# Kernel tuning notes

Measured on AMD Instinct MI355X. Metric: run time of the kernel, lower is better.

The kernel has to match this reference:

```python
import jax, jax.numpy as jnp
import numpy as np

EPS = 1e-5  # torch InstanceNorm2d default eps

def conv1x1(x, w, b):
    # x: [B,C,H,W], w: [O,C], b: [O]
    return jnp.einsum('bchw,oc->bohw', x, w) + b[None, :, None, None]

def instance_norm(x):
    # InstanceNorm2d(affine=False): normalize per-sample, per-channel over H,W
    mean = jnp.mean(x, axis=(2, 3), keepdims=True)
    var = jnp.var(x, axis=(2, 3), keepdims=True)
    return (x - mean) * jax.lax.rsqrt(var + EPS)

def proj(x, w, b):
    return jax.nn.relu(instance_norm(conv1x1(x, w, b)))

def setup_inputs() -> dict:
    key = jax.random.key(0)
    ks = jax.random.split(key, 9)
    B, C, Ci, H, W = 16, 256, 128, 64, 64
    s_in = 1.0 / np.sqrt(C)
    s_mid = 1.0 / np.sqrt(Ci)
    return {
        'x': jax.random.normal(ks[0], (B, C, H, W), jnp.float32),
        'g_w': jax.random.normal(ks[1], (Ci, C), jnp.float32) * s_in,
        'g_b': jax.random.normal(ks[2], (Ci,), jnp.float32) * s_in,
        'theta_w': jax.random.normal(ks[3], (Ci, C), jnp.float32) * s_in,
        'theta_b': jax.random.normal(ks[4], (Ci,), jnp.float32) * s_in,
        'phi_w': jax.random.normal(ks[5], (Ci, C), jnp.float32) * s_in,
        'phi_b': jax.random.normal(ks[6], (Ci,), jnp.float32) * s_in,
        'W_w': jax.random.normal(ks[7], (C, Ci), jnp.float32) * s_mid,
        'W_b': jax.random.normal(ks[8], (C,), jnp.float32) * s_mid,
    }

def reference(x, g_w, g_b, theta_w, theta_b, phi_w, phi_b, W_w, W_b):
    B, C, H, W = x.shape
    Ci = g_w.shape[0]
    N = H * W
    g_x = proj(x, g_w, g_b).reshape(B, Ci, N)        # [B,Ci,N]
    theta_x = proj(x, theta_w, theta_b).reshape(B, Ci, N)
    phi_x = proj(x, phi_w, phi_b).reshape(B, Ci, N)
    # channel-attention Gram matrix [B,Ci,Ci], softmax over last dim
    f = jnp.einsum('bin,bjn->bij', theta_x, phi_x)
    attn = jax.nn.softmax(f, axis=2)
    y = jnp.einsum('bij,bjn->bin', attn, g_x)        # [B,Ci,N]
    # replicate torch permute(0,2,1).contiguous().view(B,Ci,H,W)
    y = jnp.transpose(y, (0, 2, 1)).reshape(B, Ci, H, W)
    y = instance_norm(conv1x1(y, W_w, W_b))
    return y + x
```

## Files before the change

kernel.cpp:

```cpp
#include <hip/hip_runtime.h>

#define DEVINL __device__ __forceinline__

typedef __attribute__((ext_vector_type(8))) short bf8v;
typedef __attribute__((ext_vector_type(4))) float f32x4;
typedef __attribute__((ext_vector_type(8))) unsigned short us8;
typedef __attribute__((ext_vector_type(4))) unsigned short us4;

DEVINL unsigned short f2bf(float f) {
  unsigned int u = __builtin_bit_cast(unsigned int, f);
  u += 0x7fffu + ((u >> 16) & 1u);
  return (unsigned short)(u >> 16);
}
DEVINL unsigned short f2bf_trunc(float f) {
  return (unsigned short)(__builtin_bit_cast(unsigned int, f) >> 16);
}
DEVINL float bf2f(unsigned short h) {
  unsigned int u = ((unsigned int)h) << 16;
  return __builtin_bit_cast(float, u);
}

__global__ __launch_bounds__(512, 2)
void proj_gemm(const unsigned short* __restrict__ wall_hi,
               const unsigned short* __restrict__ wall_lo,
               const float* __restrict__ x,
               unsigned short* __restrict__ zr_hi, unsigned short* __restrict__ zr_lo,
               float* __restrict__ partials)
{
  __shared__ __align__(16) unsigned short As_hi[384 * 72];
  __shared__ __align__(16) unsigned short As_lo[256 * 72];
  __shared__ __align__(16) unsigned short Bs_hi[128 * 72];
  __shared__ __align__(16) unsigned short Bs_lo[128 * 72];

  const int t = threadIdx.x;
  const int lane = t & 63;
  const int wave = t >> 6;
  const int wm = wave >> 1, wn = wave & 1;
  const int lr = lane & 15, lk = lane >> 4;
  const int b = blockIdx.z;
  const int bx = blockIdx.x;
  const int nbase = bx * 128;
  const float* xs = x + (long)b * 256 * 4096;

  const int nl = t & 127, cg = t >> 7;
  float xv[16];

  f32x4 acc[6][4];
#pragma unroll
  for (int i = 0; i < 6; ++i)
#pragma unroll
    for (int j = 0; j < 4; ++j) acc[i][j] = (f32x4)0.0f;

#pragma unroll
  for (int i = 0; i < 16; ++i)
    xv[i] = xs[(long)(cg * 16 + i) * 4096 + nbase + nl];

  for (int kt = 0; kt < 4; ++kt) {
    const int k0 = kt * 64;
#pragma unroll
    for (int i = 0; i < 6; ++i) {
      const int q = i * 512 + t;
      const int row = q >> 3, c = q & 7;
      *(us8*)&As_hi[row * 72 + c * 8] = *(const us8*)&wall_hi[(long)row * 256 + k0 + c * 8];
    }
#pragma unroll
    for (int i = 0; i < 4; ++i) {
      const int q = i * 512 + t;
      const int row = q >> 3, c = q & 7;
      *(us8*)&As_lo[row * 72 + c * 8] = *(const us8*)&wall_lo[(long)row * 256 + k0 + c * 8];
    }
#pragma unroll
    for (int ch = 0; ch < 2; ++ch) {
      us8 h8, l8;
#pragma unroll
      for (int e = 0; e < 8; ++e) {
        const float v = xv[ch * 8 + e];
        const unsigned short hb = f2bf(v);
        h8[e] = hb;
        l8[e] = f2bf_trunc(v - bf2f(hb));
      }
      *(us8*)&Bs_hi[nl * 72 + cg * 16 + ch * 8] = h8;
      *(us8*)&Bs_lo[nl * 72 + cg * 16 + ch * 8] = l8;
    }
    __syncthreads();

    if (kt < 3) {
      const int kn = (kt + 1) * 64;
#pragma unroll
      for (int i = 0; i < 16; ++i)
        xv[i] = xs[(long)(kn + cg * 16 + i) * 4096 + nbase + nl];
    }

#pragma unroll
    for (int ks = 0; ks < 2; ++ks) {
      const int ko = ks * 32 + lk * 8;
      bf8v bh[4], bl[4];
#pragma unroll
      for (int ni = 0; ni < 4; ++ni) {
        const int r = (wn * 64 + ni * 16 + lr) * 72 + ko;
        bh[ni] = *(const bf8v*)&Bs_hi[r];
        bl[ni] = *(const bf8v*)&Bs_lo[r];
      }
#pragma unroll
      for (int mi = 0; mi < 6; ++mi) {
        const int fr = mi * 4 + wm;
        const int r = (fr * 16 + lr) * 72 + ko;
        const bf8v ah = *(const bf8v*)&As_hi[r];
        if (fr < 16) {
          const bf8v al = *(const bf8v*)&As_lo[r];
#pragma unroll
          for (int ni = 0; ni < 4; ++ni) {
            acc[mi][ni] = __builtin_amdgcn_mfma_f32_16x16x32_bf16(bh[ni], ah, acc[mi][ni], 0, 0, 0);
            acc[mi][ni] = __builtin_amdgcn_mfma_f32_16x16x32_bf16(bl[ni], ah, acc[mi][ni], 0, 0, 0);
            acc[mi][ni] = __builtin_amdgcn_mfma_f32_16x16x32_bf16(bh[ni], al, acc[mi][ni], 0, 0, 0);
          }
        } else {
#pragma unroll
          for (int ni = 0; ni < 4; ++ni)
            acc[mi][ni] = __builtin_amdgcn_mfma_f32_16x16x32_bf16(bh[ni], ah, acc[mi][ni], 0, 0, 0);
        }
      }
    }
    __syncthreads();
  }

  float* sbuf = (float*)As_hi;
#pragma unroll
  for (int mi = 0; mi < 6; ++mi) {
    float s = 0.f, ss = 0.f;
#pragma unroll
    for (int ni = 0; ni < 4; ++ni)
#pragma unroll
      for (int r = 0; r < 4; ++r) {
        const float v = acc[mi][ni][r];
        s += v; ss += v * v;
      }
    const int fr = mi * 4 + wm;
    const int slot = ((fr * 16 + lr) * 8 + (wn * 4 + lk)) * 2;
    sbuf[slot] = s; sbuf[slot + 1] = ss;
  }
  __syncthreads();
  if (t < 384) {
    float s = 0.f, ss = 0.f;
#pragma unroll
    for (int w = 0; w < 8; ++w) {
      s += sbuf[(t * 8 + w) * 2];
      ss += sbuf[(t * 8 + w) * 2 + 1];
    }
    const long pidx = ((long)bx * 6144 + b * 384 + t) * 2;
    partials[pidx] = s; partials[pidx + 1] = ss;
  }

#pragma unroll
  for (int mi = 0; mi < 6; ++mi)
#pragma unroll
    for (int ni = 0; ni < 4; ++ni) {
      const int gm = (mi * 4 + wm) * 16 + lr;
      const int gn = nbase + wn * 64 + ni * 16 + lk * 4;
      const long o = ((long)b * 384 + gm) * 4096 + gn;
      us4 hv, lv;
#pragma unroll
      for (int r = 0; r < 4; ++r) {
        const float v = acc[mi][ni][r];
        const unsigned short h = f2bf(v);
        hv[r] = h;
        lv[r] = f2bf_trunc(v - bf2f(h));
      }
      *(us4*)&zr_hi[o] = hv;
      if (gm < 256) *(us4*)&zr_lo[o] = lv;
    }
}

__global__ __launch_bounds__(256)
void stats_reduce(const float* __restrict__ partials, float* __restrict__ stats)
{
  const int row = blockIdx.x * 256 + threadIdx.x;
  float s = 0.f, ss = 0.f;
#pragma unroll
  for (int k = 0; k < 32; ++k) {
    s += partials[((long)k * 6144 + row) * 2];
    ss += partials[((long)k * 6144 + row) * 2 + 1];
  }
  const float mean = s * (1.f / 4096.f);
  const float var = ss * (1.f / 4096.f) - mean * mean;
  const float rs = rsqrtf(fmaxf(var, 0.f) + 1e-5f);
  stats[row * 2] = rs;
  stats[row * 2 + 1] = -mean * rs;
}

__global__ __launch_bounds__(256, 4)
void fgemm_norm(const unsigned short* __restrict__ zr_hi, const unsigned short* __restrict__ zr_lo,
                const float* __restrict__ stats, float* __restrict__ fpart)
{
  __shared__ __align__(16) unsigned short As_hi[128 * 72];
  __shared__ __align__(16) unsigned short As_lo[128 * 72];
  __shared__ __align__(16) unsigned short Bs_hi[128 * 72];
  __shared__ __align__(16) unsigned short Bs_lo[128 * 72];

  const int t = threadIdx.x;
  const int lane = t & 63;
  const int wave = t >> 6;
  const int wm = wave >> 1, wn = wave & 1;
  const int lr = lane & 15, lk = lane >> 4;
  const int zb = blockIdx.z >> 5, z1 = blockIdx.z & 31;
  const int koff = z1 * 128;

  f32x4 acc[4][4];
#pragma unroll
  for (int i = 0; i < 4; ++i)
#pragma unroll
    for (int j = 0; j < 4; ++j) acc[i][j] = (f32x4)0.0f;

  for (int kt = 0; kt < 2; ++kt) {
    const int k0 = koff + kt * 64;
#pragma unroll
    for (int i = 0; i < 4; ++i) {
      const int q = i * 256 + t;
      const int row = q >> 3, c = q & 7;
#pragma unroll
      for (int op = 0; op < 2; ++op) {
        const int grow = zb * 384 + op * 128 + row;
        const long g = (long)grow * 4096 + k0 + c * 8;
        const us8 h = *(const us8*)&zr_hi[g];
        const us8 l = *(const us8*)&zr_lo[g];
        const float rs = stats[grow * 2];
        const float nmrs = stats[grow * 2 + 1];
        us8 oh, ol;
#pragma unroll
        for (int e = 0; e < 8; ++e) {
          const float v = bf2f(h[e]) + bf2f(l[e]);
          const float nv = fmaxf(__builtin_fmaf(v, rs, nmrs), 0.f);
          const unsigned short hb = f2bf(nv);
          oh[e] = hb;
          ol[e] = f2bf_trunc(nv - bf2f(hb));
        }
        unsigned short* dh = op ? Bs_hi : As_hi;
        unsigned short* dl = op ? Bs_lo : As_lo;
        *(us8*)&dh[row * 72 + c * 8] = oh;
        *(us8*)&dl[row * 72 + c * 8] = ol;
      }
    }
    __syncthreads();
#pragma unroll
    for (int ks = 0; ks < 2; ++ks) {
      const int ko = ks * 32 + lk * 8;
      bf8v ah[4], bh[4], al[4], bl[4];
#pragma unroll
      for (int mi = 0; mi < 4; ++mi) {
        const int r = (wm * 64 + mi * 16 + lr) * 72 + ko;
        ah[mi] = *(const bf8v*)&As_hi[r];
        al[mi] = *(const bf8v*)&As_lo[r];
      }
#pragma unroll
      for (int ni = 0; ni < 4; ++ni) {
        const int r = (wn * 64 + ni * 16 + lr) * 72 + ko;
        bh[ni] = *(const bf8v*)&Bs_hi[r];
        bl[ni] = *(const bf8v*)&Bs_lo[r];
      }
#pragma unroll
      for (int mi = 0; mi < 4; ++mi)
#pragma unroll
        for (int ni = 0; ni < 4; ++ni) {
          acc[mi][ni] = __builtin_amdgcn_mfma_f32_16x16x32_bf16(bh[ni], ah[mi], acc[mi][ni], 0, 0, 0);
          acc[mi][ni] = __builtin_amdgcn_mfma_f32_16x16x32_bf16(bl[ni], ah[mi], acc[mi][ni], 0, 0, 0);
          acc[mi][ni] = __builtin_amdgcn_mfma_f32_16x16x32_bf16(bh[ni], al[mi], acc[mi][ni], 0, 0, 0);
        }
    }
    __syncthreads();
  }

  const long cOff = ((long)zb * 32 + z1) * 16384;
#pragma unroll
  for (int mi = 0; mi < 4; ++mi)
#pragma unroll
    for (int ni = 0; ni < 4; ++ni) {
      const int gm = wm * 64 + mi * 16 + lr;
      const int gn = wn * 64 + ni * 16 + lk * 4;
      *(f32x4*)&fpart[cOff + (long)gm * 128 + gn] = acc[mi][ni];
    }
}

__global__ __launch_bounds__(256, 2)
void gemm_y(const unsigned short* __restrict__ Ah0, const unsigned short* __restrict__ Bh0,
            unsigned short* __restrict__ Cout,
            int lda, int ldb, int ldc, int ksteps, int z1count,
            long aS1, long aS2, long bS1, long bS2, long cS1, long cS2)
{
  __shared__ __align__(16) unsigned short As_hi[128 * 72];
  __shared__ __align__(16) unsigned short Bs_hi[128 * 72];

  const int t = threadIdx.x;
  const int lane = t & 63;
  const int wave = t >> 6;
  const int wm = wave >> 1, wn = wave & 1;
  const int lr = lane & 15, lk = lane >> 4;

  const int z = blockIdx.z;
  const int zb = z / z1count, z1 = z - zb * z1count;
  const unsigned short* Ah = Ah0 + zb * aS2 + z1 * aS1;
  const unsigned short* Bh = Bh0 + zb * bS2 + z1 * bS1;
  const long cOff = zb * cS2 + z1 * cS1;

  f32x4 acc[4][4];
#pragma unroll
  for (int i = 0; i < 4; ++i)
#pragma unroll
    for (int j = 0; j < 4; ++j) acc[i][j] = (f32x4)0.0f;

  for (int kt = 0; kt < ksteps; ++kt) {
    const int k0 = kt * 64;
#pragma unroll
    for (int i = 0; i < 4; ++i) {
      const int q = i * 256 + t;
      const int row = q >> 3, c = q & 7;
      const int lo = row * 72 + c * 8;
      *(us8*)&As_hi[lo] = *(const us8*)&Ah[(long)row * lda + k0 + c * 8];
      *(us8*)&Bs_hi[lo] = *(const us8*)&Bh[(long)row * ldb + k0 + c * 8];
    }
    __syncthreads();
#pragma unroll
    for (int ks = 0; ks < 2; ++ks) {
      const int ko = ks * 32 + lk * 8;
      bf8v ah[4], bh[4];
#pragma unroll
      for (int mi = 0; mi < 4; ++mi)
        ah[mi] = *(const bf8v*)&As_hi[(wm * 64 + mi * 16 + lr) * 72 + ko];
#pragma unroll
      for (int ni = 0; ni < 4; ++ni)
        bh[ni] = *(const bf8v*)&Bs_hi[(wn * 64 + ni * 16 + lr) * 72 + ko];
#pragma unroll
      for (int mi = 0; mi < 4; ++mi)
#pragma unroll
        for (int ni = 0; ni < 4; ++ni)
          acc[mi][ni] = __builtin_amdgcn_mfma_f32_16x16x32_bf16(bh[ni], ah[mi], acc[mi][ni], 0, 0, 0);
    }
    __syncthreads();
  }

#pragma unroll
  for (int mi = 0; mi < 4; ++mi)
#pragma unroll
    for (int ni = 0; ni < 4; ++ni) {
      const int gm = wm * 64 + mi * 16 + lr;
      const int gn = wn * 64 + ni * 16 + lk * 4;
      const f32x4 v = acc[mi][ni];
      us4 o;
#pragma unroll
      for (int r = 0; r < 4; ++r) o[r] = f2bf(v[r]);
      *(us4*)&Cout[cOff + (long)gm * ldc + gn] = o;
    }
}

__global__ __launch_bounds__(256, 2)
void conv2_gemm(const unsigned short* __restrict__ w2h,
                const unsigned short* __restrict__ y4T,
                unsigned short* __restrict__ z2b)
{
  __shared__ __align__(16) unsigned short As_hi[256 * 72];
  __shared__ __align__(16) unsigned short Bs_hi[128 * 72];

  const int t = threadIdx.x;
  const int lane = t & 63;
  const int wave = t >> 6;
  const int wm = wave >> 1, wn = wave & 1;
  const int lr = lane & 15, lk = lane >> 4;
  const int b = blockIdx.z;
  const int nbase = blockIdx.x * 128;
  const unsigned short* Bh = y4T + (long)b * 4096 * 128 + (long)nbase * 128;

  f32x4 acc[8][4];
#pragma unroll
  for (int i = 0; i < 8; ++i)
#pragma unroll
    for (int j = 0; j < 4; ++j) acc[i][j] = (f32x4)0.0f;

  for (int kt = 0; kt < 2; ++kt) {
    const int k0 = kt * 64;
#pragma unroll
    for (int i = 0; i < 8; ++i) {
      const int q = i * 256 + t;
      const int row = q >> 3, c = q & 7;
      *(us8*)&As_hi[row * 72 + c * 8] = *(const us8*)&w2h[(long)row * 128 + k0 + c * 8];
    }
#pragma unroll
    for (int i = 0; i < 4; ++i) {
      const int q = i * 256 + t;
      const int row = q >> 3, c = q & 7;
      *(us8*)&Bs_hi[row * 72 + c * 8] = *(const us8*)&Bh[(long)row * 128 + k0 + c * 8];
    }
    __syncthreads();
#pragma unroll
    for (int ks = 0; ks < 2; ++ks) {
      const int ko = ks * 32 + lk * 8;
      bf8v ah[8], bh[4];
#pragma unroll
      for (int mi = 0; mi < 8; ++mi)
        ah[mi] = *(const bf8v*)&As_hi[(wm * 128 + mi * 16 + lr) * 72 + ko];
#pragma unroll
      for (int ni = 0; ni < 4; ++ni)
        bh[ni] = *(const bf8v*)&Bs_hi[(wn * 64 + ni * 16 + lr) * 72 + ko];
#pragma unroll
      for (int mi = 0; mi < 8; ++mi)
#pragma unroll
        for (int ni = 0; ni < 4; ++ni)
          acc[mi][ni] = __builtin_amdgcn_mfma_f32_16x16x32_bf16(bh[ni], ah[mi], acc[mi][ni], 0, 0, 0);
    }
    __syncthreads();
  }

#pragma unroll
  for (int mi = 0; mi < 8; ++mi)
#pragma unroll
    for (int ni = 0; ni < 4; ++ni) {
      const int gm = wm * 128 + mi * 16 + lr;
      const int gn = nbase + wn * 64 + ni * 16 + lk * 4;
      const f32x4 v = acc[mi][ni];
      us4 o;
#pragma unroll
      for (int r = 0; r < 4; ++r) o[r] = f2bf(v[r]);
      *(us4*)&z2b[((long)b * 256 + gm) * 4096 + gn] = o;
    }
}

__global__ __launch_bounds__(256)
void prep_weights(const float* __restrict__ g_w, const float* __restrict__ th_w,
                  const float* __restrict__ ph_w, const float* __restrict__ W_w,
                  unsigned short* __restrict__ wall_hi, unsigned short* __restrict__ wall_lo,
                  unsigned short* __restrict__ w2h)
{
  const int i = blockIdx.x * 256 + threadIdx.x;
  float v;
  if (i < 32768) v = th_w[i];
  else if (i < 65536) v = ph_w[i - 32768];
  else v = g_w[i - 65536];
  const unsigned short h = f2bf(v);
  wall_hi[i] = h;
  if (i < 65536) wall_lo[i] = f2bf_trunc(v - bf2f(h));
  if (i < 32768) w2h[i] = f2bf(W_w[i]);
}

__global__ __launch_bounds__(256)
void norm_transpose_g(const unsigned short* __restrict__ zr_hi,
                      const float* __restrict__ stats,
                      unsigned short* __restrict__ gT)
{
  __shared__ unsigned short T[64 * 136];
  const int b = blockIdx.y, n0 = blockIdx.x * 64;
  const int t = threadIdx.x;
  const int c = t >> 1, part = t & 1;
  const int grow = b * 384 + 256 + c;
  const float rs = stats[grow * 2];
  const float nmrs = stats[grow * 2 + 1];
  const long off = (long)grow * 4096 + n0 + part * 32;
#pragma unroll
  for (int j = 0; j < 4; ++j) {
    const us8 h = *(const us8*)&zr_hi[off + j * 8];
#pragma unroll
    for (int e = 0; e < 8; ++e) {
      const float v = bf2f(h[e]);
      const float nv = fmaxf(__builtin_fmaf(v, rs, nmrs), 0.f);
      T[(part * 32 + j * 8 + e) * 136 + c] = f2bf(nv);
    }
  }
  __syncthreads();
  const int nl = t >> 2, q = t & 3;
  const long obase = ((long)b * 4096 + n0 + nl) * 128 + q * 32;
#pragma unroll
  for (int k = 0; k < 4; ++k) {
    us8 o;
#pragma unroll
    for (int e = 0; e < 8; ++e) o[e] = T[nl * 136 + q * 32 + k * 8 + e];
    *(us8*)&gT[obase + k * 8] = o;
  }
}

__global__ __launch_bounds__(64)
void softmax_attn(const float* __restrict__ fpart, unsigned short* __restrict__ attn)
{
  const int row = blockIdx.x;
  const int b = row >> 7, i = row & 127;
  const int t = threadIdx.x;
  float v0 = 0.f, v1 = 0.f;
#pragma unroll
  for (int kc = 0; kc < 32; ++kc) {
    const float* p = fpart + ((long)(b * 32 + kc)) * 16384 + i * 128;
    v0 += p[t];
    v1 += p[t + 64];
  }
  float mx = fmaxf(v0, v1);
  for (int o = 32; o > 0; o >>= 1) mx = fmaxf(mx, __shfl_xor(mx, o));
  const float e0 = __expf(v0 - mx), e1 = __expf(v1 - mx);
  float s = e0 + e1;
  for (int o = 32; o > 0; o >>= 1) s += __shfl_xor(s, o);
  const float inv = 1.f / s;
  attn[(long)row * 128 + t] = f2bf(e0 * inv);
  attn[(long)row * 128 + t + 64] = f2bf(e1 * inv);
}

__global__ __launch_bounds__(256)
void finalize(const unsigned short* __restrict__ z2b, const float* __restrict__ x,
              float* __restrict__ out)
{
  const int row = blockIdx.x;
  const long base = (long)row * 4096;
  const int t = threadIdx.x;
  float v[16];
  float s = 0.f, ss = 0.f;
#pragma unroll
  for (int h = 0; h < 2; ++h) {
    us8 u = *(const us8*)&z2b[base + t * 16 + h * 8];
#pragma unroll
    for (int e = 0; e < 8; ++e) {
      const float f = bf2f(u[e]);
      v[h * 8 + e] = f;
      s += f; ss += f * f;
    }
  }
  __shared__ float r0[256], r1[256];
  r0[t] = s; r1[t] = ss;
  __syncthreads();
  for (int o = 128; o > 0; o >>= 1) {
    if (t < o) { r0[t] += r0[t + o]; r1[t] += r1[t + o]; }
    __syncthreads();
  }
  const float mean = r0[0] * (1.f / 4096.f);
  const float var = r1[0] * (1.f / 4096.f) - mean * mean;
  const float rs = rsqrtf(fmaxf(var, 0.f) + 1e-5f);
#pragma unroll
  for (int i = 0; i < 4; ++i) {
    f32x4 xr = *(const f32x4*)&x[base + t * 16 + i * 4];
    f32x4 o;
#pragma unroll
    for (int e = 0; e < 4; ++e) o[e] = (v[i * 4 + e] - mean) * rs + xr[e];
    *(f32x4*)&out[base + t * 16 + i * 4] = o;
  }
}

extern "C" void kernel_launch(void* const* d_in, const int* in_sizes, int n_in,
                              void* d_out, int out_size, void* d_ws, size_t ws_size,
                              hipStream_t stream)
{
  const float* x    = (const float*)d_in[0];
  const float* g_w  = (const float*)d_in[1];
  const float* th_w = (const float*)d_in[3];
  const float* ph_w = (const float*)d_in[5];
  const float* W_w  = (const float*)d_in[7];

  char* ws = (char*)d_ws;
  const size_t MB = 1024ull * 1024ull;
  if (ws_size < 186 * MB) return;

  unsigned short* zr_hi    = (unsigned short*)(ws);
  unsigned short* zr_lo    = (unsigned short*)(ws + 48 * MB);
  float*          fpart    = (float*)(ws + 96 * MB);
  unsigned short* attn     = (unsigned short*)(ws + 128 * MB);
  unsigned short* gT       = (unsigned short*)(ws + 132 * MB);
  unsigned short* y4T      = (unsigned short*)(ws + 148 * MB);
  unsigned short* z2b      = (unsigned short*)(ws);
  float*          partials = (float*)(ws + 164 * MB);
  float*          stats    = (float*)(ws + 167 * MB);
  unsigned short* wall_hi  = (unsigned short*)(ws + 168 * MB);
  unsigned short* wall_lo  = (unsigned short*)(ws + 168 * MB + 256 * 1024);
  unsigned short* w2h      = (unsigned short*)(ws + 168 * MB + 512 * 1024);

  prep_weights<<<dim3(384), 256, 0, stream>>>(g_w, th_w, ph_w, W_w, wall_hi, wall_lo, w2h);

  proj_gemm<<<dim3(32, 1, 16), 512, 0, stream>>>(wall_hi, wall_lo, x, zr_hi, zr_lo, partials);

  stats_reduce<<<dim3(24), 256, 0, stream>>>(partials, stats);

  norm_transpose_g<<<dim3(64, 16), 256, 0, stream>>>(zr_hi, stats, gT);

  fgemm_norm<<<dim3(1, 1, 512), 256, 0, stream>>>(zr_hi, zr_lo, stats, fpart);

  softmax_attn<<<dim3(2048), 64, 0, stream>>>(fpart, attn);

  gemm_y<<<dim3(1, 1, 512), 256, 0, stream>>>(
      attn, gT, y4T,
      128, 4096, 128, 2, 32,
      0, 16384, 128, (long)4096 * 128, 16384, (long)4096 * 128);

  conv2_gemm<<<dim3(32, 1, 16), 256, 0, stream>>>(w2h, y4T, z2b);

  finalize<<<dim3(4096), 256, 0, stream>>>(z2b, x, (float*)d_out);
}
```

Before: 160.8 us.

## Switch split-precision pipeline from bf16 to fp16 and compact lo-buffer layout

Replaces every bf16 hi/lo split and bf16 MFMA with fp16 equivalents across all GEMM kernels, using hardware float-to-half conversion instead of manual rounding bit tricks. The lo buffer of the projection output now holds only the 256 rows that need it, which shrinks the workspace and the traffic for that buffer. The software prefetch of x in proj_gemm is dropped in favour of loading inside each k-step, and fgemm_norm's launch-bounds occupancy hint drops from 4 to 2. fp16 has a narrower range than bf16, so pre-normalisation activations or logits could overflow. Losing the prefetch may also expose global-load latency.

```diff
diff --git a/kernel.cpp b/kernel.cpp
--- a/kernel.cpp
+++ b/kernel.cpp
@@ -2,35 +2,29 @@
 
 #define DEVINL __device__ __forceinline__
 
-typedef __attribute__((ext_vector_type(8))) short bf8v;
+typedef __attribute__((ext_vector_type(8))) _Float16 h8v;
 typedef __attribute__((ext_vector_type(4))) float f32x4;
 typedef __attribute__((ext_vector_type(8))) unsigned short us8;
 typedef __attribute__((ext_vector_type(4))) unsigned short us4;
 
-DEVINL unsigned short f2bf(float f) {
-  unsigned int u = __builtin_bit_cast(unsigned int, f);
-  u += 0x7fffu + ((u >> 16) & 1u);
-  return (unsigned short)(u >> 16);
-}
-DEVINL unsigned short f2bf_trunc(float f) {
-  return (unsigned short)(__builtin_bit_cast(unsigned int, f) >> 16);
-}
-DEVINL float bf2f(unsigned short h) {
-  unsigned int u = ((unsigned int)h) << 16;
-  return __builtin_bit_cast(float, u);
+DEVINL unsigned short f2h(float f) {
+  return __builtin_bit_cast(unsigned short, (_Float16)f);
+}
+DEVINL float h2f(unsigned short u) {
+  return (float)__builtin_bit_cast(_Float16, u);
 }
 
 __global__ __launch_bounds__(512, 2)
-void proj_gemm(const unsigned short* __restrict__ wall_hi,
-               const unsigned short* __restrict__ wall_lo,
+void proj_gemm(const unsigned short* __restrict__ wall_h,
+               const unsigned short* __restrict__ wall_l,
                const float* __restrict__ x,
-               unsigned short* __restrict__ zr_hi, unsigned short* __restrict__ zr_lo,
+               unsigned short* __restrict__ zh, unsigned short* __restrict__ zl,
                float* __restrict__ partials)
 {
-  __shared__ __align__(16) unsigned short As_hi[384 * 72];
-  __shared__ __align__(16) unsigned short As_lo[256 * 72];
-  __shared__ __align__(16) unsigned short Bs_hi[128 * 72];
-  __shared__ __align__(16) unsigned short Bs_lo[128 * 72];
+  __shared__ __align__(16) unsigned short As_h[384 * 72];
+  __shared__ __align__(16) unsigned short As_l[256 * 72];
+  __shared__ __align__(16) unsigned short Bs_h[128 * 72];
+  __shared__ __align__(16) unsigned short Bs_l[128 * 72];
 
   const int t = threadIdx.x;
   const int lane = t & 63;
@@ -42,18 +36,13 @@
   const int nbase = bx * 128;
   const float* xs = x + (long)b * 256 * 4096;
 
+  f32x4 acc[6][4];
+#pragma unroll
+  for (int i = 0; i < 6; ++i)
+#pragma unroll
+    for (int j = 0; j < 4; ++j) acc[i][j] = (f32x4)0.0f;
+
   const int nl = t & 127, cg = t >> 7;
-  float xv[16];
-
-  f32x4 acc[6][4];
-#pragma unroll
-  for (int i = 0; i < 6; ++i)
-#pragma unroll
-    for (int j = 0; j < 4; ++j) acc[i][j] = (f32x4)0.0f;
-
-#pragma unroll
-  for (int i = 0; i < 16; ++i)
-    xv[i] = xs[(long)(cg * 16 + i) * 4096 + nbase + nl];
 
   for (int kt = 0; kt < 4; ++kt) {
     const int k0 = kt * 64;
@@ -61,70 +50,65 @@
     for (int i = 0; i < 6; ++i) {
       const int q = i * 512 + t;
       const int row = q >> 3, c = q & 7;
-      *(us8*)&As_hi[row * 72 + c * 8] = *(const us8*)&wall_hi[(long)row * 256 + k0 + c * 8];
+      *(us8*)&As_h[row * 72 + c * 8] = *(const us8*)&wall_h[(long)row * 256 + k0 + c * 8];
     }
 #pragma unroll
     for (int i = 0; i < 4; ++i) {
       const int q = i * 512 + t;
       const int row = q >> 3, c = q & 7;
-      *(us8*)&As_lo[row * 72 + c * 8] = *(const us8*)&wall_lo[(long)row * 256 + k0 + c * 8];
-    }
-#pragma unroll
-    for (int ch = 0; ch < 2; ++ch) {
+      *(us8*)&As_l[row * 72 + c * 8] = *(const us8*)&wall_l[(long)row * 256 + k0 + c * 8];
+    }
+#pragma unroll
+    for (int hp = 0; hp < 2; ++hp) {
+      float xv[8];
+#pragma unroll
+      for (int i = 0; i < 8; ++i)
+        xv[i] = xs[(long)(k0 + cg * 16 + hp * 8 + i) * 4096 + nbase + nl];
       us8 h8, l8;
 #pragma unroll
       for (int e = 0; e < 8; ++e) {
-        const float v = xv[ch * 8 + e];
-        const unsigned short hb = f2bf(v);
+        const unsigned short hb = f2h(xv[e]);
         h8[e] = hb;
-        l8[e] = f2bf_trunc(v - bf2f(hb));
-      }
-      *(us8*)&Bs_hi[nl * 72 + cg * 16 + ch * 8] = h8;
-      *(us8*)&Bs_lo[nl * 72 + cg * 16 + ch * 8] = l8;
-    }
-    __syncthreads();
-
-    if (kt < 3) {
-      const int kn = (kt + 1) * 64;
-#pragma unroll
-      for (int i = 0; i < 16; ++i)
-        xv[i] = xs[(long)(kn + cg * 16 + i) * 4096 + nbase + nl];
-    }
+        l8[e] = f2h(xv[e] - h2f(hb));
+      }
+      *(us8*)&Bs_h[nl * 72 + cg * 16 + hp * 8] = h8;
+      *(us8*)&Bs_l[nl * 72 + cg * 16 + hp * 8] = l8;
+    }
+    __syncthreads();
 
 #pragma unroll
     for (int ks = 0; ks < 2; ++ks) {
       const int ko = ks * 32 + lk * 8;
-      bf8v bh[4], bl[4];
+      h8v bh[4], bl[4];
 #pragma unroll
       for (int ni = 0; ni < 4; ++ni) {
         const int r = (wn * 64 + ni * 16 + lr) * 72 + ko;
-        bh[ni] = *(const bf8v*)&Bs_hi[r];
-        bl[ni] = *(const bf8v*)&Bs_lo[r];
+        bh[ni] = *(const h8v*)&Bs_h[r];
+        bl[ni] = *(const h8v*)&Bs_l[r];
       }
 #pragma unroll
       for (int mi = 0; mi < 6; ++mi) {
         const int fr = mi * 4 + wm;
-        const int r = (fr * 16 + lr) * 72 + ko;
-        const bf8v ah = *(const bf8v*)&As_hi[r];
+        const h8v ah = *(const h8v*)&As_h[(fr * 16 + lr) * 72 + ko];
         if (fr < 16) {
-          const bf8v al = *(const bf8v*)&As_lo[r];
+          const h8v al = *(const h8v*)&As_l[(fr * 16 + lr) * 72 + ko];
 #pragma unroll
           for (int ni = 0; ni < 4; ++ni) {
-            acc[mi][ni] = __builtin_amdgcn_mfma_f32_16x16x32_bf16(bh[ni], ah, acc[mi][ni], 0, 0, 0);
-            acc[mi][ni] = __builtin_amdgcn_mfma_f32_16x16x32_bf16(bl[ni], ah, acc[mi][ni], 0, 0, 0);
-            acc[mi][ni] = __builtin_amdgcn_mfma_f32_16x16x32_bf16(bh[ni], al, acc[mi][ni], 0, 0, 0);
+            acc[mi][ni] = __builtin_amdgcn_mfma_f32_16x16x32_f16(bh[ni], ah, acc[mi][ni], 0, 0, 0);
+            acc[mi][ni] = __builtin_amdgcn_mfma_f32_16x16x32_f16(bl[ni], ah, acc[mi][ni], 0, 0, 0);
+            acc[mi][ni] = __builtin_amdgcn_mfma_f32_16x16x32_f16(bh[ni], al, acc[mi][ni], 0, 0, 0);
           }
         } else {
 #pragma unroll
           for (int ni = 0; ni < 4; ++ni)
-            acc[mi][ni] = __builtin_amdgcn_mfma_f32_16x16x32_bf16(bh[ni], ah, acc[mi][ni], 0, 0, 0);
+            acc[mi][ni] = __builtin_amdgcn_mfma_f32_16x16x32_f16(bh[ni], ah, acc[mi][ni], 0, 0, 0);
         }
       }
     }
     __syncthreads();
   }
 
-  float* sbuf = (float*)As_hi;
+  float* sbuf = (float*)As_h;
 #pragma unroll
   for (int mi = 0; mi < 6; ++mi) {
     float s = 0.f, ss = 0.f;
@@ -157,17 +141,16 @@
     for (int ni = 0; ni < 4; ++ni) {
       const int gm = (mi * 4 + wm) * 16 + lr;
       const int gn = nbase + wn * 64 + ni * 16 + lk * 4;
-      const long o = ((long)b * 384 + gm) * 4096 + gn;
       us4 hv, lv;
 #pragma unroll
       for (int r = 0; r < 4; ++r) {
         const float v = acc[mi][ni][r];
-        const unsigned short h = f2bf(v);
+        const unsigned short h = f2h(v);
         hv[r] = h;
-        lv[r] = f2bf_trunc(v - bf2f(h));
-      }
-      *(us4*)&zr_hi[o] = hv;
-      if (gm < 256) *(us4*)&zr_lo[o] = lv;
+        lv[r] = f2h(v - h2f(h));
+      }
+      *(us4*)&zh[((long)b * 384 + gm) * 4096 + gn] = hv;
+      if (gm < 256) *(us4*)&zl[((long)b * 256 + gm) * 4096 + gn] = lv;
     }
 }
 
@@ -188,14 +171,14 @@
   stats[row * 2 + 1] = -mean * rs;
 }
 
-__global__ __launch_bounds__(256, 4)
-void fgemm_norm(const unsigned short* __restrict__ zr_hi, const unsigned short* __restrict__ zr_lo,
+__global__ __launch_bounds__(256, 2)
+void fgemm_norm(const unsigned short* __restrict__ zh, const unsigned short* __restrict__ zl,
                 const float* __restrict__ stats, float* __restrict__ fpart)
 {
-  __shared__ __align__(16) unsigned short As_hi[128 * 72];
-  __shared__ __align__(16) unsigned short As_lo[128 * 72];
-  __shared__ __align__(16) unsigned short Bs_hi[128 * 72];
-  __shared__ __align__(16) unsigned short Bs_lo[128 * 72];
+  __shared__ __align__(16) unsigned short As_h[128 * 72];
+  __shared__ __align__(16) unsigned short As_l[128 * 72];
+  __shared__ __align__(16) unsigned short Bs_h[128 * 72];
+  __shared__ __align__(16) unsigned short Bs_l[128 * 72];
 
   const int t = threadIdx.x;
   const int lane = t & 63;
@@ -219,23 +202,23 @@
       const int row = q >> 3, c = q & 7;
 #pragma unroll
       for (int op = 0; op < 2; ++op) {
-        const int grow = zb * 384 + op * 128 + row;
-        const long g = (long)grow * 4096 + k0 + c * 8;
-        const us8 h = *(const us8*)&zr_hi[g];
-        const us8 l = *(const us8*)&zr_lo[g];
-        const float rs = stats[grow * 2];
-        const float nmrs = stats[grow * 2 + 1];
+        const int zrow = op * 128 + row;
+        const us8 h = *(const us8*)&zh[((long)zb * 384 + zrow) * 4096 + k0 + c * 8];
+        const us8 l = *(const us8*)&zl[((long)zb * 256 + zrow) * 4096 + k0 + c * 8];
+        const int srow = zb * 384 + zrow;
+        const float rs = stats[srow * 2];
+        const float nmrs = stats[srow * 2 + 1];
         us8 oh, ol;
 #pragma unroll
         for (int e = 0; e < 8; ++e) {
-          const float v = bf2f(h[e]) + bf2f(l[e]);
+          const float v = h2f(h[e]) + h2f(l[e]);
           const float nv = fmaxf(__builtin_fmaf(v, rs, nmrs), 0.f);
-          const unsigned short hb = f2bf(nv);
+          const unsigned short hb = f2h(nv);
           oh[e] = hb;
-          ol[e] = f2bf_trunc(nv - bf2f(hb));
+          ol[e] = f2h(nv - h2f(hb));
         }
-        unsigned short* dh = op ? Bs_hi : As_hi;
-        unsigned short* dl = op ? Bs_lo : As_lo;
+        unsigned short* dh = op ? Bs_h : As_h;
+        unsigned short* dl = op ? Bs_l : As_l;
         *(us8*)&dh[row * 72 + c * 8] = oh;
         *(us8*)&dl[row * 72 + c * 8] = ol;
       }
@@ -244,26 +227,26 @@
 #pragma unroll
     for (int ks = 0; ks < 2; ++ks) {
       const int ko = ks * 32 + lk * 8;
-      bf8v ah[4], bh[4], al[4], bl[4];
+      h8v ah[4], bh[4], al[4], bl[4];
 #pragma unroll
       for (int mi = 0; mi < 4; ++mi) {
         const int r = (wm * 64 + mi * 16 + lr) * 72 + ko;
-        ah[mi] = *(const bf8v*)&As_hi[r];
-        al[mi] = *(const bf8v*)&As_lo[r];
+        ah[mi] = *(const h8v*)&As_h[r];
+        al[mi] = *(const h8v*)&As_l[r];
       }
 #pragma unroll
       for (int ni = 0; ni < 4; ++ni) {
         const int r = (wn * 64 + ni * 16 + lr) * 72 + ko;
-        bh[ni] = *(const bf8v*)&Bs_hi[r];
-        bl[ni] = *(const bf8v*)&Bs_lo[r];
+        bh[ni] = *(const h8v*)&Bs_h[r];
+        bl[ni] = *(const h8v*)&Bs_l[r];
       }
 #pragma unroll
       for (int mi = 0; mi < 4; ++mi)
 #pragma unroll
         for (int ni = 0; ni < 4; ++ni) {
-          acc[mi][ni] = __builtin_amdgcn_mfma_f32_16x16x32_bf16(bh[ni], ah[mi], acc[mi][ni], 0, 0, 0);
-          acc[mi][ni] = __builtin_amdgcn_mfma_f32_16x16x32_bf16(bl[ni], ah[mi], acc[mi][ni], 0, 0, 0);
-          acc[mi][ni] = __builtin_amdgcn_mfma_f32_16x16x32_bf16(bh[ni], al[mi], acc[mi][ni], 0, 0, 0);
+          acc[mi][ni] = __builtin_amdgcn_mfma_f32_16x16x32_f16(bh[ni], ah[mi], acc[mi][ni], 0, 0, 0);
+          acc[mi][ni] = __builtin_amdgcn_mfma_f32_16x16x32_f16(bl[ni], ah[mi], acc[mi][ni], 0, 0, 0);
+          acc[mi][ni] = __builtin_amdgcn_mfma_f32_16x16x32_f16(bh[ni], al[mi], acc[mi][ni], 0, 0, 0);
         }
     }
     __syncthreads();
@@ -286,8 +269,8 @@
             int lda, int ldb, int ldc, int ksteps, int z1count,
             long aS1, long aS2, long bS1, long bS2, long cS1, long cS2)
 {
-  __shared__ __align__(16) unsigned short As_hi[128 * 72];
-  __shared__ __align__(16) unsigned short Bs_hi[128 * 72];
+  __shared__ __align__(16) unsigned short As[128 * 72];
+  __shared__ __align__(16) unsigned short Bs[128 * 72];
 
   const int t = threadIdx.x;
   const int lane = t & 63;
@@ -314,25 +297,25 @@
       const int q = i * 256 + t;
       const int row = q >> 3, c = q & 7;
       const int lo = row * 72 + c * 8;
-      *(us8*)&As_hi[lo] = *(const us8*)&Ah[(long)row * lda + k0 + c * 8];
-      *(us8*)&Bs_hi[lo] = *(const us8*)&Bh[(long)row * ldb + k0 + c * 8];
+      *(us8*)&As[lo] = *(const us8*)&Ah[(long)row * lda + k0 + c * 8];
+      *(us8*)&Bs[lo] = *(const us8*)&Bh[(long)row * ldb + k0 + c * 8];
     }
     __syncthreads();
 #pragma unroll
     for (int ks = 0; ks < 2; ++ks) {
       const int ko = ks * 32 + lk * 8;
-      bf8v ah[4], bh[4];
+      h8v ah[4], bh[4];
 #pragma unroll
       for (int mi = 0; mi < 4; ++mi)
-        ah[mi] = *(const bf8v*)&As_hi[(wm * 64 + mi * 16 + lr) * 72 + ko];
+        ah[mi] = *(const h8v*)&As[(wm * 64 + mi * 16 + lr) * 72 + ko];
 #pragma unroll
       for (int ni = 0; ni < 4; ++ni)
-        bh[ni] = *(const bf8v*)&Bs_hi[(wn * 64 + ni * 16 + lr) * 72 + ko];
+        bh[ni] = *(const h8v*)&Bs[(wn * 64 + ni * 16 + lr) * 72 + ko];
 #pragma unroll
       for (int mi = 0; mi < 4; ++mi)
 #pragma unroll
         for (int ni = 0; ni < 4; ++ni)
-          acc[mi][ni] = __builtin_amdgcn_mfma_f32_16x16x32_bf16(bh[ni], ah[mi], acc[mi][ni], 0, 0, 0);
+          acc[mi][ni] = __builtin_amdgcn_mfma_f32_16x16x32_f16(bh[ni], ah[mi], acc[mi][ni], 0, 0, 0);
     }
     __syncthreads();
   }
@@ -346,7 +329,7 @@
       const f32x4 v = acc[mi][ni];
       us4 o;
 #pragma unroll
-      for (int r = 0; r < 4; ++r) o[r] = f2bf(v[r]);
+      for (int r = 0; r < 4; ++r) o[r] = f2h(v[r]);
       *(us4*)&Cout[cOff + (long)gm * ldc + gn] = o;
     }
 }
@@ -356,8 +339,8 @@
                 const unsigned short* __restrict__ y4T,
                 unsigned short* __restrict__ z2b)
 {
-  __shared__ __align__(16) unsigned short As_hi[256 * 72];
-  __shared__ __align__(16) unsigned short Bs_hi[128 * 72];
+  __shared__ __align__(16) unsigned short As[256 * 72];
+  __shared__ __align__(16) unsigned short Bs[128 * 72];
 
   const int t = threadIdx.x;
   const int lane = t & 63;
@@ -380,30 +363,30 @@
     for (int i = 0; i < 8; ++i) {
       const int q = i * 256 + t;
       const int row = q >> 3, c = q & 7;
-      *(us8*)&As_hi[row * 72 + c * 8] = *(const us8*)&w2h[(long)row * 128 + k0 + c * 8];
+      *(us8*)&As[row * 72 + c * 8] = *(const us8*)&w2h[(long)row * 128 + k0 + c * 8];
     }
 #pragma unroll
     for (int i = 0; i < 4; ++i) {
       const int q = i * 256 + t;
       const int row = q >> 3, c = q & 7;
-      *(us8*)&Bs_hi[row * 72 + c * 8] = *(const us8*)&Bh[(long)row * 128 + k0 + c * 8];
+      *(us8*)&Bs[row * 72 + c * 8] = *(const us8*)&Bh[(long)row * 128 + k0 + c * 8];
     }
     __syncthreads();
 #pragma unroll
     for (int ks = 0; ks < 2; ++ks) {
       const int ko = ks * 32 + lk * 8;
-      bf8v ah[8], bh[4];
+      h8v ah[8], bh[4];
 #pragma unroll
       for (int mi = 0; mi < 8; ++mi)
-        ah[mi] = *(const bf8v*)&As_hi[(wm * 128 + mi * 16 + lr) * 72 + ko];
+        ah[mi] = *(const h8v*)&As[(wm * 128 + mi * 16 + lr) * 72 + ko];
 #pragma unroll
       for (int ni = 0; ni < 4; ++ni)
-        bh[ni] = *(const bf8v*)&Bs_hi[(wn * 64 + ni * 16 + lr) * 72 + ko];
+        bh[ni] = *(const h8v*)&Bs[(wn * 64 + ni * 16 + lr) * 72 + ko];
 #pragma unroll
       for (int mi = 0; mi < 8; ++mi)
 #pragma unroll
         for (int ni = 0; ni < 4; ++ni)
-          acc[mi][ni] = __builtin_amdgcn_mfma_f32_16x16x32_bf16(bh[ni], ah[mi], acc[mi][ni], 0, 0, 0);
+          acc[mi][ni] = __builtin_amdgcn_mfma_f32_16x16x32_f16(bh[ni], ah[mi], acc[mi][ni], 0, 0, 0);
     }
     __syncthreads();
   }
@@ -417,7 +400,7 @@
       const f32x4 v = acc[mi][ni];
       us4 o;
 #pragma unroll
-      for (int r = 0; r < 4; ++r) o[r] = f2bf(v[r]);
+      for (int r = 0; r < 4; ++r) o[r] = f2h(v[r]);
       *(us4*)&z2b[((long)b * 256 + gm) * 4096 + gn] = o;
     }
 }
@@ -425,7 +408,7 @@
 __global__ __launch_bounds__(256)
 void prep_weights(const float* __restrict__ g_w, const float* __restrict__ th_w,
                   const float* __restrict__ ph_w, const float* __restrict__ W_w,
-                  unsigned short* __restrict__ wall_hi, unsigned short* __restrict__ wall_lo,
+                  unsigned short* __restrict__ wall_h, unsigned short* __restrict__ wall_l,
                   unsigned short* __restrict__ w2h)
 {
   const int i = blockIdx.x * 256 + threadIdx.x;
@@ -433,14 +416,14 @@
   if (i < 32768) v = th_w[i];
   else if (i < 65536) v = ph_w[i - 32768];
   else v = g_w[i - 65536];
-  const unsigned short h = f2bf(v);
-  wall_hi[i] = h;
-  if (i < 65536) wall_lo[i] = f2bf_trunc(v - bf2f(h));
-  if (i < 32768) w2h[i] = f2bf(W_w[i]);
+  const unsigned short h = f2h(v);
+  wall_h[i] = h;
+  if (i < 65536) wall_l[i] = f2h(v - h2f(h));
+  if (i < 32768) w2h[i] = f2h(W_w[i]);
 }
 
 __global__ __launch_bounds__(256)
-void norm_transpose_g(const unsigned short* __restrict__ zr_hi,
+void norm_transpose_g(const unsigned short* __restrict__ zh,
                       const float* __restrict__ stats,
                       unsigned short* __restrict__ gT)
 {
@@ -454,12 +437,11 @@
   const long off = (long)grow * 4096 + n0 + part * 32;
 #pragma unroll
   for (int j = 0; j < 4; ++j) {
-    const us8 h = *(const us8*)&zr_hi[off + j * 8];
+    const us8 h = *(const us8*)&zh[off + j * 8];
 #pragma unroll
     for (int e = 0; e < 8; ++e) {
-      const float v = bf2f(h[e]);
-      const float nv = fmaxf(__builtin_fmaf(v, rs, nmrs), 0.f);
-      T[(part * 32 + j * 8 + e) * 136 + c] = f2bf(nv);
+      const float nv = fmaxf(__builtin_fmaf(h2f(h[e]), rs, nmrs), 0.f);
+      T[(part * 32 + j * 8 + e) * 136 + c] = f2h(nv);
     }
   }
   __syncthreads();
@@ -493,8 +475,8 @@
   float s = e0 + e1;
   for (int o = 32; o > 0; o >>= 1) s += __shfl_xor(s, o);
   const float inv = 1.f / s;
-  attn[(long)row * 128 + t] = f2bf(e0 * inv);
-  attn[(long)row * 128 + t + 64] = f2bf(e1 * inv);
+  attn[(long)row * 128 + t] = f2h(e0 * inv);
+  attn[(long)row * 128 + t + 64] = f2h(e1 * inv);
 }
 
 __global__ __launch_bounds__(256)
@@ -511,7 +493,7 @@
     us8 u = *(const us8*)&z2b[base + t * 16 + h * 8];
 #pragma unroll
     for (int e = 0; e < 8; ++e) {
-      const float f = bf2f(u[e]);
+      const float f = h2f(u[e]);
       v[h * 8 + e] = f;
       s += f; ss += f * f;
     }
@@ -550,28 +532,28 @@
   const size_t MB = 1024ull * 1024ull;
   if (ws_size < 186 * MB) return;
 
-  unsigned short* zr_hi    = (unsigned short*)(ws);
-  unsigned short* zr_lo    = (unsigned short*)(ws + 48 * MB);
-  float*          fpart    = (float*)(ws + 96 * MB);
-  unsigned short* attn     = (unsigned short*)(ws + 128 * MB);
-  unsigned short* gT       = (unsigned short*)(ws + 132 * MB);
-  unsigned short* y4T      = (unsigned short*)(ws + 148 * MB);
+  unsigned short* zh       = (unsigned short*)(ws);
+  unsigned short* zl       = (unsigned short*)(ws + 51 * MB);
+  float*          fpart    = (float*)(ws + 85 * MB);
+  unsigned short* attn     = (unsigned short*)(ws + 119 * MB);
+  unsigned short* gT       = (unsigned short*)(ws + 120 * MB);
+  unsigned short* y4T      = (unsigned short*)(ws + 137 * MB);
   unsigned short* z2b      = (unsigned short*)(ws);
-  float*          partials = (float*)(ws + 164 * MB);
-  float*          stats    = (float*)(ws + 167 * MB);
-  unsigned short* wall_hi  = (unsigned short*)(ws + 168 * MB);
-  unsigned short* wall_lo  = (unsigned short*)(ws + 168 * MB + 256 * 1024);
-  unsigned short* w2h      = (unsigned short*)(ws + 168 * MB + 512 * 1024);
-
-  prep_weights<<<dim3(384), 256, 0, stream>>>(g_w, th_w, ph_w, W_w, wall_hi, wall_lo, w2h);
-
-  proj_gemm<<<dim3(32, 1, 16), 512, 0, stream>>>(wall_hi, wall_lo, x, zr_hi, zr_lo, partials);
+  float*          partials = (float*)(ws + 154 * MB);
+  float*          stats    = (float*)(ws + 158 * MB);
+  unsigned short* wall_h   = (unsigned short*)(ws + 159 * MB);
+  unsigned short* wall_l   = (unsigned short*)(ws + 159 * MB + 256 * 1024);
+  unsigned short* w2h      = (unsigned short*)(ws + 159 * MB + 512 * 1024);
+
+  prep_weights<<<dim3(384), 256, 0, stream>>>(g_w, th_w, ph_w, W_w, wall_h, wall_l, w2h);
+
+  proj_gemm<<<dim3(32, 1, 16), 512, 0, stream>>>(wall_h, wall_l, x, zh, zl, partials);
 
   stats_reduce<<<dim3(24), 256, 0, stream>>>(partials, stats);
 
-  norm_transpose_g<<<dim3(64, 16), 256, 0, stream>>>(zr_hi, stats, gT);
-
-  fgemm_norm<<<dim3(1, 1, 512), 256, 0, stream>>>(zr_hi, zr_lo, stats, fpart);
+  norm_transpose_g<<<dim3(64, 16), 256, 0, stream>>>(zh, stats, gT);
+
+  fgemm_norm<<<dim3(1, 1, 512), 256, 0, stream>>>(zh, zl, stats, fpart);
 
   softmax_attn<<<dim3(2048), 64, 0, stream>>>(fpart, attn);
 
```

Result: no change. 162.0 us (+0.7%).
